# Performance work log

Measured on AMD Instinct MI355X. Metric: run time of the kernel, lower is better.

The kernel has to match this reference:

```python
import jax, jax.numpy as jnp
import numpy as np

N_WIRES = 4
N_LAYERS = 2
B = 16384
EPS = 1e-5


def apply_ry(state, wire, theta):
    # state: (B,2,2,2,2) complex64; theta: scalar or (B,)
    st = jnp.moveaxis(state, wire + 1, 1)
    half = jnp.asarray(theta) * 0.5
    c = jnp.cos(half).reshape(-1, 1, 1, 1).astype(state.dtype)
    s = jnp.sin(half).reshape(-1, 1, 1, 1).astype(state.dtype)
    n0 = c * st[:, 0] - s * st[:, 1]
    n1 = s * st[:, 0] + c * st[:, 1]
    return jnp.moveaxis(jnp.stack([n0, n1], axis=1), 1, wire + 1)


def apply_rz(state, wire, theta):
    st = jnp.moveaxis(state, wire + 1, 1)
    half = jnp.asarray(theta) * 0.5
    c = jnp.cos(half)
    s = jnp.sin(half)
    p0 = (c - 1j * s).reshape(-1, 1, 1, 1).astype(state.dtype)
    p1 = (c + 1j * s).reshape(-1, 1, 1, 1).astype(state.dtype)
    return jnp.moveaxis(jnp.stack([p0 * st[:, 0], p1 * st[:, 1]], axis=1), 1, wire + 1)


def apply_cnot(state, ctrl, tgt):
    st = jnp.moveaxis(state, (ctrl + 1, tgt + 1), (1, 2))
    # flip target where control == 1
    st = jnp.concatenate([st[:, :1], st[:, 1:, ::-1]], axis=1)
    return jnp.moveaxis(st, (1, 2), (ctrl + 1, tgt + 1))


def expect_z(state):
    probs = jnp.real(state * jnp.conj(state))  # (B,2,2,2,2)
    exps = []
    for w in range(N_WIRES):
        p = jnp.moveaxis(probs, w + 1, 1)
        exps.append((p[:, 0] - p[:, 1]).sum(axis=(1, 2, 3)))
    return jnp.stack(exps, axis=-1)  # (B,4)


def quanv(x, qparams):
    bsz = x.shape[0]
    # 2x2 patches in row-major loop order: (B, 196, 4) with [p00,p01,p10,p11]
    patches = x.reshape(bsz, 14, 2, 14, 2).transpose(0, 1, 3, 2, 4).reshape(bsz, 196, 4)
    patches = jnp.transpose(patches, (1, 0, 2))  # (196, B, 4)
    state0 = jnp.zeros((bsz, 2, 2, 2, 2), jnp.complex64).at[:, 0, 0, 0, 0].set(1.0)

    def step(state, vals):
        # NOTE: original code never resets the device between patches -> state carries over
        for i in range(N_WIRES):
            state = apply_ry(state, i, vals[:, i])
        for l in range(N_LAYERS):
            for i in range(N_WIRES):
                state = apply_ry(state, i, qparams[l, i, 0])
                state = apply_rz(state, i, qparams[l, i, 1])
            for i in range(N_WIRES - 1):
                state = apply_cnot(state, i, i + 1)
        return state, expect_z(state)

    _, meas = jax.lax.scan(step, state0, patches)  # (196, B, 4)
    return jnp.transpose(meas, (1, 0, 2)).reshape(bsz, 196 * 4)


def batchnorm(h, g, b):
    # training-mode BatchNorm1d: biased batch statistics
    m = h.mean(axis=0)
    v = h.var(axis=0)
    return g * (h - m) / jnp.sqrt(v + EPS) + b


def setup_inputs() -> dict:
    key = jax.random.key(0)
    ks = jax.random.split(key, 6)
    x = jax.random.uniform(ks[0], (B, 28, 28), dtype=jnp.float32)
    qparams = jax.random.normal(ks[1], (N_LAYERS, N_WIRES, 2), dtype=jnp.float32)
    w1 = jax.random.normal(ks[2], (256, 784), dtype=jnp.float32) * 0.03
    w2 = jax.random.normal(ks[3], (256, 256), dtype=jnp.float32) * 0.05
    w3 = jax.random.normal(ks[4], (10, 256), dtype=jnp.float32) * 0.05
    return {
        "x": x, "qparams": qparams,
        "w1": w1, "b1": jnp.zeros((256,), jnp.float32),
        "g1": jnp.ones((256,), jnp.float32), "be1": jnp.zeros((256,), jnp.float32),
        "w2": w2, "b2": jnp.zeros((256,), jnp.float32),
        "g2": jnp.ones((256,), jnp.float32), "be2": jnp.zeros((256,), jnp.float32),
        "w3": w3, "b3": jnp.zeros((10,), jnp.float32),
    }


def reference(x, qparams, w1, b1, g1, be1, w2, b2, g2, be2, w3, b3):
    feats = quanv(x, qparams)                      # (B, 784)
    h = jax.nn.relu(batchnorm(feats @ w1.T + b1, g1, be1))
    h2 = jax.nn.relu(batchnorm(h @ w2.T + b2, g2, be2)) + h
    return jax.nn.log_softmax(h2 @ w3.T + b3, axis=-1)
```

## Files before the change

kernel.cpp:

```cpp
#include <hip/hip_runtime.h>
#include <math.h>

#define BQ 16384
#define KFP 800
#define NH 256
#define NCLS 10

typedef float f32x2 __attribute__((ext_vector_type(2)));
typedef float f32x4 __attribute__((ext_vector_type(4)));
typedef unsigned int u32x2 __attribute__((ext_vector_type(2)));
typedef __bf16 bf16x8 __attribute__((ext_vector_type(8)));
typedef __bf16 bf16x4 __attribute__((ext_vector_type(4)));


template<int ST>
__device__ __forceinline__ void u_ry(float* sr, float* si, float c, float s) {
#pragma unroll
  for (int i = 0; i < 16; i++) {
    if (i & ST) continue;
    const int j = i | ST;
    const float a0r = sr[i], a0i = si[i], a1r = sr[j], a1i = si[j];
    sr[i] = c * a0r - s * a1r;  si[i] = c * a0i - s * a1i;
    sr[j] = s * a0r + c * a1r;  si[j] = s * a0i + c * a1i;
  }
}
template<int ST>
__device__ __forceinline__ void u_rz(float* sr, float* si, float c, float s) {
#pragma unroll
  for (int i = 0; i < 16; i++) {
    const float pz = (i & ST) ? s : -s;
    const float ar = sr[i], ai = si[i];
    sr[i] = c * ar - pz * ai;
    si[i] = c * ai + pz * ar;
  }
}
template<int SC, int STG>
__device__ __forceinline__ void u_cnot(float* sr, float* si) {
#pragma unroll
  for (int i = 0; i < 16; i++) {
    if (!(i & SC) || (i & STG)) continue;
    const int j = i | STG;
    float t;
    t = sr[i]; sr[i] = sr[j]; sr[j] = t;
    t = si[i]; si[i] = si[j]; si[j] = t;
  }
}

__global__ __launch_bounds__(256) void build_U(const float* __restrict__ qp,
                                               __bf16* __restrict__ Abuf) {
  __shared__ float Ur[16][16], Ui[16][16];
  const int tid = threadIdx.x;
  if (tid < 16) {
    float sr[16], si[16];
#pragma unroll
    for (int i = 0; i < 16; i++) { sr[i] = (i == tid) ? 1.f : 0.f; si[i] = 0.f; }
#pragma unroll
    for (int l = 0; l < 2; l++) {
      { const float t = qp[l*8 + 0] * 0.5f; u_ry<8>(sr, si, cosf(t), sinf(t)); }
      { const float t = qp[l*8 + 1] * 0.5f; u_rz<8>(sr, si, cosf(t), sinf(t)); }
      { const float t = qp[l*8 + 2] * 0.5f; u_ry<4>(sr, si, cosf(t), sinf(t)); }
      { const float t = qp[l*8 + 3] * 0.5f; u_rz<4>(sr, si, cosf(t), sinf(t)); }
      { const float t = qp[l*8 + 4] * 0.5f; u_ry<2>(sr, si, cosf(t), sinf(t)); }
      { const float t = qp[l*8 + 5] * 0.5f; u_rz<2>(sr, si, cosf(t), sinf(t)); }
      { const float t = qp[l*8 + 6] * 0.5f; u_ry<1>(sr, si, cosf(t), sinf(t)); }
      { const float t = qp[l*8 + 7] * 0.5f; u_rz<1>(sr, si, cosf(t), sinf(t)); }
      u_cnot<8, 4>(sr, si);
      u_cnot<4, 2>(sr, si);
      u_cnot<2, 1>(sr, si);
    }
#pragma unroll
    for (int r = 0; r < 16; r++) { Ur[r][tid] = sr[r]; Ui[r][tid] = si[r]; }
  }
  __syncthreads();
  for (int f = tid; f < 2048; f += 256) {
    const int m   = f & 7;
    const int row = (f >> 3) & 15;
    const int kg  = (f >> 7) & 3;
    const int hl  = (f >> 9) & 1;
    const int t   = (f >> 10) & 1;
    const int k   = kg * 8 + m;
    const int ri_o  = (row >> 2) & 1;
    const int amp_o = ((row >> 3) & 1) * 8 + t * 4 + (row & 3);
    const int ri_i  = (k >> 3) & 1;
    const int amp_i = ((k >> 4) & 1) * 8 + (m >> 2) * 4 + (m & 3);
    const float u_r = Ur[amp_o][amp_i], u_i = Ui[amp_o][amp_i];
    float v = (ri_o == 0) ? ((ri_i == 0) ? u_r : -u_i)
                          : ((ri_i == 0) ? u_i : u_r);
    if (hl) {
      const __bf16 hb = (__bf16)v;
      v = v - (float)hb;
    }
    Abuf[f] = (__bf16)v;
  }
}


__device__ __forceinline__ float swz16(float v) {
  return __int_as_float(__builtin_amdgcn_ds_swizzle(__float_as_int(v), 0x401F));
}
__device__ __forceinline__ float pl32(float v, bool r0sel) {
  const u32x2 r = __builtin_amdgcn_permlane32_swap(
      __float_as_uint(v), __float_as_uint(v), false, false);
  return __uint_as_float(r0sel ? r.x : r.y);
}

__global__ __launch_bounds__(256) void quanv_mfma(
    const float* __restrict__ x, const __bf16* __restrict__ Abuf,
    __bf16* __restrict__ feats) {
  const int tid = threadIdx.x;
  const int l = tid & 63;
  const int wv = tid >> 6;
  const int col = l & 15;
  const int kg = l >> 4;
  const int b = blockIdx.x * 64 + wv * 16 + col;
  const float* xb = x + (size_t)b * 784;
  __bf16* fb = feats + (size_t)b * KFP;
  const float sg0 = (l & 32) ? 1.f : -1.f;

  const u32x2 pt = __builtin_amdgcn_permlane32_swap((unsigned)l, (unsigned)l,
                                                    false, false);
  const bool p32r0 = (pt.x == (unsigned)(l ^ 32));

  const bf16x8* Ab = (const bf16x8*)Abuf;
  const bf16x8 A0h = Ab[(0 * 4 + kg) * 16 + col];
  const bf16x8 A0l = Ab[(1 * 4 + kg) * 16 + col];
  const bf16x8 A1h = Ab[(2 * 4 + kg) * 16 + col];
  const bf16x8 A1l = Ab[(3 * 4 + kg) * 16 + col];

  f32x4 c0 = {(kg == 0) ? 1.f : 0.f, 0.f, 0.f, 0.f};
  f32x4 c1 = {0.f, 0.f, 0.f, 0.f};
  const f32x4 z4 = {0.f, 0.f, 0.f, 0.f};

  auto meas = [&](__bf16* dst) {
    const float sq0 = c0.x * c0.x, sq1 = c0.y * c0.y;
    const float sq2 = c0.z * c0.z, sq3 = c0.w * c0.w;
    const float sq4 = c1.x * c1.x, sq5 = c1.y * c1.y;
    const float sq6 = c1.z * c1.z, sq7 = c1.w * c1.w;
    const float s01 = sq0 + sq1, s23 = sq2 + sq3;
    const float s45 = sq4 + sq5, s67 = sq6 + sq7;
    const float d01 = sq0 - sq1, d23 = sq2 - sq3;
    const float d45 = sq4 - sq5, d67 = sq6 - sq7;
    const float z3 = (d01 + d23) + (d45 + d67);
    const float z2 = (s01 - s23) + (s45 - s67);
    const float q03 = s01 + s23, q47 = s45 + s67;
    const float z1 = q03 - q47;
    const float T  = q03 + q47;
    const float z3a = z3 + swz16(z3);
    const float z2a = z2 + swz16(z2);
    const float z1a = z1 + swz16(z1);
    const float Ta  = T + swz16(T);
    const float z3f = z3a + pl32(z3a, p32r0);
    const float z2f = z2a + pl32(z2a, p32r0);
    const float z1f = z1a + pl32(z1a, p32r0);
    const float z0f = sg0 * (pl32(Ta, p32r0) - Ta);
    if (kg == 0) {
      bf16x4 o = {(__bf16)z0f, (__bf16)z1f, (__bf16)z2f, (__bf16)z3f};
      *(bf16x4*)dst = o;
    }
  };

  auto step = [&](float2 t0, float2 t1) {
    const float h0 = t0.x * 0.5f, h1 = t0.y * 0.5f;
    const float h2 = t1.x * 0.5f, h3 = t1.y * 0.5f;
    const float cw0 = __cosf(h0), sw0 = __sinf(h0);
    const float cw1 = __cosf(h1), sw1 = __sinf(h1);
    const float cw2 = __cosf(h2), sw2 = __sinf(h2);
    const float cw3 = __cosf(h3), sw3 = __sinf(h3);

    float S[8] = {c0.x, c0.y, c0.z, c0.w, c1.x, c1.y, c1.z, c1.w};
#pragma unroll
    for (int j = 0; j < 4; j++) {
      const float a = S[j];
      S[j]     = fmaf(-sw1, S[4 + j], cw1 * S[j]);
      S[4 + j] = fmaf( sw1, a,        cw1 * S[4 + j]);
    }
#pragma unroll
    for (int base = 0; base < 8; base += 4)
#pragma unroll
      for (int j = 0; j < 2; j++) {
        const int i0 = base + j, i1 = base + j + 2;
        const float a = S[i0];
        S[i0] = fmaf(-sw2, S[i1], cw2 * S[i0]);
        S[i1] = fmaf( sw2, a,     cw2 * S[i1]);
      }
#pragma unroll
    for (int i0 = 0; i0 < 8; i0 += 2) {
      const float a = S[i0];
      S[i0]     = fmaf(-sw3, S[i0 + 1], cw3 * S[i0]);
      S[i0 + 1] = fmaf( sw3, a,         cw3 * S[i0 + 1]);
    }
    float P[8];
#pragma unroll
    for (int i = 0; i < 8; i++) P[i] = pl32(S[i], p32r0);
    const float ss0 = sg0 * sw0;
#pragma unroll
    for (int i = 0; i < 8; i++) S[i] = fmaf(ss0, P[i], cw0 * S[i]);

    bf16x8 Bh, Bl;
#pragma unroll
    for (int i = 0; i < 8; i++) {
      const __bf16 hb = (__bf16)S[i];
      Bh[i] = hb;
      Bl[i] = (__bf16)(S[i] - (float)hb);
    }

    f32x4 p0 = __builtin_amdgcn_mfma_f32_16x16x32_bf16(A0h, Bh, z4, 0, 0, 0);
    f32x4 q0 = __builtin_amdgcn_mfma_f32_16x16x32_bf16(A0l, Bh, z4, 0, 0, 0);
    q0 = __builtin_amdgcn_mfma_f32_16x16x32_bf16(A0h, Bl, q0, 0, 0, 0);
    f32x4 p1 = __builtin_amdgcn_mfma_f32_16x16x32_bf16(A1h, Bh, z4, 0, 0, 0);
    f32x4 q1 = __builtin_amdgcn_mfma_f32_16x16x32_bf16(A1l, Bh, z4, 0, 0, 0);
    q1 = __builtin_amdgcn_mfma_f32_16x16x32_bf16(A1h, Bl, q1, 0, 0, 0);
    c0 = p0 + q0;
    c1 = p1 + q1;
  };

  float2 t0 = *(const float2*)(xb);
  float2 t1 = *(const float2*)(xb + 28);
  int nrr = 0, ncc = 0;
  {
    const float2 n0 = *(const float2*)(xb + 2);
    const float2 n1 = *(const float2*)(xb + 30);
    step(t0, t1);
    t0 = n0; t1 = n1; ncc = 1; nrr = 0;
  }
  for (int it = 1; it < 196; ++it) {
    int nc = ncc + 1, nr = nrr;
    if (nc == 14) { nc = 0; nr = nrr + 1; }
    const float* np = (it < 195) ? (xb + (2 * nr) * 28 + 2 * nc) : xb;
    const float2 n0 = *(const float2*)np;
    const float2 n1 = *(const float2*)(np + 28);

    meas(fb + (it - 1) * 4);
    step(t0, t1);

    t0 = n0; t1 = n1; ncc = nc; nrr = nr;
  }
  meas(fb + 195 * 4);

  if (kg == 0) {
    *(uint4*)(fb + 784) = (uint4){0, 0, 0, 0};
    *(uint4*)(fb + 792) = (uint4){0, 0, 0, 0};
  }
}

#define GBM 128
#define GBN 64
#define GBK 32

__device__ __forceinline__ void gld16(const void* g, void* l) {
  __builtin_amdgcn_global_load_lds(
      (const __attribute__((address_space(1))) unsigned int*)g,
      (__attribute__((address_space(3))) unsigned int*)l, 16, 0, 0);
}

__global__ __launch_bounds__(256) void gemm_bf16_nt(
    const __bf16* __restrict__ A, const __bf16* __restrict__ B,
    const float* __restrict__ bias, float* __restrict__ C,
    int M, int N, int K) {
  __shared__ char lds[24576];
  const int tid = threadIdx.x;
  const int bm = blockIdx.x * GBM;
  const int bn = blockIdx.y * GBN;
  const int NK = K / GBK;
  const size_t lda = (size_t)K * 2;

  const int srow = tid >> 2;
  const int lc16 = tid & 3;
  const int ag0 = lc16 ^ ((srow >> 1) & 3);
  const int ag1 = lc16 ^ (((srow + 64) >> 1) & 3);
  const char* a0p = (const char*)A + (size_t)(bm + srow) * lda + ag0 * 16;
  const char* a1p = (const char*)A + (size_t)(bm + 64 + srow) * lda + ag1 * 16;
  const char* b0p = (const char*)B + (size_t)(bn + srow) * lda + ag0 * 16;

  const int wid = tid >> 6, lane = tid & 63;
  const int wr = wid >> 1, wc = wid & 1;
  const int ln15 = lane & 15, ln4 = lane >> 4;
  int aoff[4], boff[2];
#pragma unroll
  for (int m = 0; m < 4; m++) {
    const int row = wr * 64 + m * 16 + ln15;
    aoff[m] = row * 64 + ((ln4 ^ ((row >> 1) & 3)) * 16);
  }
#pragma unroll
  for (int n = 0; n < 2; n++) {
    const int row = wc * 32 + n * 16 + ln15;
    boff[n] = 16384 + row * 64 + ((ln4 ^ ((row >> 1) & 3)) * 16);
  }

  f32x4 acc[4][2];
#pragma unroll
  for (int m = 0; m < 4; m++)
#pragma unroll
    for (int n = 0; n < 2; n++) acc[m][n] = (f32x4){0.f, 0.f, 0.f, 0.f};

  auto stage = [&](int buf, int kt) {
    const size_t kb = (size_t)kt * GBK * 2;
    char* as = lds + buf * 8192 + tid * 16;
    char* bs = lds + 16384 + buf * 4096 + tid * 16;
    gld16(a0p + kb, as);
    gld16(a1p + kb, as + 4096);
    gld16(b0p + kb, bs);
  };

  stage(0, 0);
  for (int kt = 0; kt < NK; kt++) {
    __syncthreads();
    if (kt + 1 < NK) stage((kt + 1) & 1, kt + 1);
    const int ab = (kt & 1) * 8192, bb = (kt & 1) * 4096;
    bf16x8 af[4], bfr[2];
#pragma unroll
    for (int m = 0; m < 4; m++) af[m] = *(const bf16x8*)(lds + ab + aoff[m]);
#pragma unroll
    for (int n = 0; n < 2; n++) bfr[n] = *(const bf16x8*)(lds + bb + boff[n]);
#pragma unroll
    for (int m = 0; m < 4; m++)
#pragma unroll
      for (int n = 0; n < 2; n++)
        acc[m][n] = __builtin_amdgcn_mfma_f32_16x16x32_bf16(af[m], bfr[n], acc[m][n], 0, 0, 0);
  }

#pragma unroll
  for (int n = 0; n < 2; n++) {
    const int ccol = bn + wc * 32 + n * 16 + ln15;
    const float bv = bias[ccol];
#pragma unroll
    for (int m = 0; m < 4; m++) {
      const int crow = bm + wr * 64 + m * 16 + ln4 * 4;
#pragma unroll
      for (int r = 0; r < 4; r++)
        C[(size_t)(crow + r) * N + ccol] = acc[m][n][r] + bv;
    }
  }
}

__global__ __launch_bounds__(256) void cvt_pad_w1(const float* __restrict__ w,
                                                  __bf16* __restrict__ o) {
  const int r = blockIdx.x;
  for (int c = threadIdx.x; c < KFP; c += 256)
    o[r * KFP + c] = (c < 784) ? (__bf16)w[r * 784 + c] : (__bf16)0.f;
}
__global__ __launch_bounds__(256) void cvt_w2(const float* __restrict__ w,
                                              __bf16* __restrict__ o) {
  const int i = blockIdx.x * 256 + threadIdx.x;
  o[i] = (__bf16)w[i];
}

__global__ __launch_bounds__(256) void bn_partial(const float* __restrict__ h,
                                                  float* __restrict__ partial) {
  const int blk = blockIdx.x;
  const int t = threadIdx.x;
  const float* p = h + (size_t)blk * 64 * NH + t;
  float s = 0.f, ss = 0.f;
#pragma unroll 4
  for (int r = 0; r < 64; r++) {
    const float v = p[(size_t)r * NH];
    s += v; ss += v * v;
  }
  partial[blk * 512 + t] = s;
  partial[blk * 512 + 256 + t] = ss;
}

__global__ __launch_bounds__(256) void bn_finalize(
    const float* __restrict__ partial, const float* __restrict__ g,
    const float* __restrict__ be, float* __restrict__ ab, float* __restrict__ cb) {
  const int t = threadIdx.x;
  float s = 0.f, ss = 0.f;
  for (int i = 0; i < 256; i++) {
    s += partial[i * 512 + t];
    ss += partial[i * 512 + 256 + t];
  }
  const float mean = s * (1.f / 16384.f);
  const float var = ss * (1.f / 16384.f) - mean * mean;
  const float rstd = rsqrtf(var + 1e-5f);
  const float a = g[t] * rstd;
  ab[t] = a;
  cb[t] = be[t] - mean * a;
}

__global__ __launch_bounds__(256) void bn_relu(float* __restrict__ h,
                                               __bf16* __restrict__ hb,
                                               const float* __restrict__ ab,
                                               const float* __restrict__ cb) {
  const size_t i = (size_t)blockIdx.x * 256 + threadIdx.x;
  float4 v = ((float4*)h)[i];
  const int col = (int)((i * 4) & (NH - 1));
  const float4 a = *(const float4*)(ab + col);
  const float4 c = *(const float4*)(cb + col);
  v.x = fmaxf(v.x * a.x + c.x, 0.f);
  v.y = fmaxf(v.y * a.y + c.y, 0.f);
  v.z = fmaxf(v.z * a.z + c.z, 0.f);
  v.w = fmaxf(v.w * a.w + c.w, 0.f);
  ((float4*)h)[i] = v;
  bf16x4 o = {(__bf16)v.x, (__bf16)v.y, (__bf16)v.z, (__bf16)v.w};
  *(bf16x4*)(hb + i * 4) = o;
}

__global__ __launch_bounds__(256) void bn_relu_res(float* __restrict__ h2,
                                                   const float* __restrict__ h1,
                                                   const float* __restrict__ ab,
                                                   const float* __restrict__ cb) {
  const size_t i = (size_t)blockIdx.x * 256 + threadIdx.x;
  float4 v = ((float4*)h2)[i];
  const float4 rsd = ((const float4*)h1)[i];
  const int col = (int)((i * 4) & (NH - 1));
  const float4 a = *(const float4*)(ab + col);
  const float4 c = *(const float4*)(cb + col);
  v.x = fmaxf(v.x * a.x + c.x, 0.f) + rsd.x;
  v.y = fmaxf(v.y * a.y + c.y, 0.f) + rsd.y;
  v.z = fmaxf(v.z * a.z + c.z, 0.f) + rsd.z;
  v.w = fmaxf(v.w * a.w + c.w, 0.f) + rsd.w;
  ((float4*)h2)[i] = v;
}

__global__ __launch_bounds__(256) void head_kernel(
    const float* __restrict__ h2, const float* __restrict__ w3,
    const float* __restrict__ b3, float* __restrict__ out) {
  __shared__ float w3s[NCLS * NH];
  for (int i = threadIdx.x; i < NCLS * NH; i += 256) w3s[i] = w3[i];
  __syncthreads();

  const int m = blockIdx.x * 256 + threadIdx.x;
  const float* hr = h2 + (size_t)m * NH;
  float acc[NCLS];
#pragma unroll
  for (int n = 0; n < NCLS; n++) acc[n] = b3[n];

  for (int k = 0; k < NH; k += 4) {
    const float4 hv = *(const float4*)(hr + k);
#pragma unroll
    for (int n = 0; n < NCLS; n++) {
      const float4 wv = *(const float4*)&w3s[n * NH + k];
      acc[n] += hv.x * wv.x + hv.y * wv.y + hv.z * wv.z + hv.w * wv.w;
    }
  }

  float mx = acc[0];
#pragma unroll
  for (int n = 1; n < NCLS; n++) mx = fmaxf(mx, acc[n]);
  float se = 0.f;
#pragma unroll
  for (int n = 0; n < NCLS; n++) se += expf(acc[n] - mx);
  const float lse = logf(se) + mx;
#pragma unroll
  for (int n = 0; n < NCLS; n++) out[(size_t)m * NCLS + n] = acc[n] - lse;
}

extern "C" void kernel_launch(void* const* d_in, const int* in_sizes, int n_in,
                              void* d_out, int out_size, void* d_ws, size_t ws_size,
                              hipStream_t stream) {
  const float* x   = (const float*)d_in[0];
  const float* qp  = (const float*)d_in[1];
  const float* w1  = (const float*)d_in[2];
  const float* b1  = (const float*)d_in[3];
  const float* g1  = (const float*)d_in[4];
  const float* be1 = (const float*)d_in[5];
  const float* w2  = (const float*)d_in[6];
  const float* b2  = (const float*)d_in[7];
  const float* g2  = (const float*)d_in[8];
  const float* be2 = (const float*)d_in[9];
  const float* w3  = (const float*)d_in[10];
  const float* b3  = (const float*)d_in[11];
  float* out = (float*)d_out;

  char* w = (char*)d_ws;
  __bf16* feats = (__bf16*)w;
  float*  h1    = (float*)(w + 26214400);
  float*  h2    = (float*)(w + 42991616);
  __bf16* h1b   = (__bf16*)(w + 59768832);
  __bf16* w1b   = (__bf16*)(w + 68157440);
  __bf16* w2b   = (__bf16*)(w + 68567040);
  float*  partial = (float*)(w + 68698112);
  float*  ab1   = (float*)(w + 69222400);
  float*  cb1   = (float*)(w + 69223424);
  float*  ab2   = (float*)(w + 69224448);
  float*  cb2   = (float*)(w + 69225472);
  __bf16* Abuf  = (__bf16*)(w + 69226496);

  build_U<<<1, 256, 0, stream>>>(qp, Abuf);
  cvt_pad_w1<<<256, 256, 0, stream>>>(w1, w1b);
  cvt_w2<<<256, 256, 0, stream>>>(w2, w2b);

  quanv_mfma<<<BQ / 64, 256, 0, stream>>>(x, Abuf, feats);

  gemm_bf16_nt<<<dim3(BQ / GBM, NH / GBN), 256, 0, stream>>>(
      feats, w1b, b1, h1, BQ, NH, KFP);
  bn_partial<<<256, 256, 0, stream>>>(h1, partial);
  bn_finalize<<<1, 256, 0, stream>>>(partial, g1, be1, ab1, cb1);
  bn_relu<<<(BQ * NH / 4) / 256, 256, 0, stream>>>(h1, h1b, ab1, cb1);

  gemm_bf16_nt<<<dim3(BQ / GBM, NH / GBN), 256, 0, stream>>>(
      h1b, w2b, b2, h2, BQ, NH, NH);
  bn_partial<<<256, 256, 0, stream>>>(h2, partial);
  bn_finalize<<<1, 256, 0, stream>>>(partial, g2, be2, ab2, cb2);
  bn_relu_res<<<(BQ * NH / 4) / 256, 256, 0, stream>>>(h2, h1, ab2, cb2);

  head_kernel<<<BQ / 256, 256, 0, stream>>>(h2, w3, b3, out);
}
```

Before: 228.8 us.

## Fuse BN statistics into GEMM epilogue, merge prep and tail kernels

Merges the three weight/unitary prep kernels into one launch and folds the batchnorm sum and sum-of-squares into the GEMM epilogue using LDS reduction plus global atomics. This removes the separate bn_partial passes over h1/h2. The second BN+ReLU, residual add and classifier head become one tail kernel that reads the bf16 h1 as the residual, so the h2 round trip is dropped. The quanv loop now computes the trig for the next patch after the current step and packs bf16 with perm instructions. Risks: atomic float accumulation makes the statistics order-dependent, and the residual now uses a bf16-rounded h1.

```diff
diff --git a/kernel.cpp b/kernel.cpp
--- a/kernel.cpp
+++ b/kernel.cpp
@@ -6,9 +6,9 @@
 #define NH 256
 #define NCLS 10
 
-typedef float f32x2 __attribute__((ext_vector_type(2)));
 typedef float f32x4 __attribute__((ext_vector_type(4)));
 typedef unsigned int u32x2 __attribute__((ext_vector_type(2)));
+typedef unsigned int u32x4 __attribute__((ext_vector_type(4)));
 typedef __bf16 bf16x8 __attribute__((ext_vector_type(8)));
 typedef __bf16 bf16x4 __attribute__((ext_vector_type(4)));
 
@@ -46,51 +46,70 @@
   }
 }
 
-__global__ __launch_bounds__(256) void build_U(const float* __restrict__ qp,
-                                               __bf16* __restrict__ Abuf) {
-  __shared__ float Ur[16][16], Ui[16][16];
+__global__ __launch_bounds__(256) void prep_kernel(
+    const float* __restrict__ qp, const float* __restrict__ w1,
+    const float* __restrict__ w2, __bf16* __restrict__ Abuf,
+    __bf16* __restrict__ w1b, __bf16* __restrict__ w2b,
+    float* __restrict__ gs1, float* __restrict__ gs2) {
+  const int bid = blockIdx.x;
   const int tid = threadIdx.x;
-  if (tid < 16) {
-    float sr[16], si[16];
-#pragma unroll
-    for (int i = 0; i < 16; i++) { sr[i] = (i == tid) ? 1.f : 0.f; si[i] = 0.f; }
-#pragma unroll
-    for (int l = 0; l < 2; l++) {
-      { const float t = qp[l*8 + 0] * 0.5f; u_ry<8>(sr, si, cosf(t), sinf(t)); }
-      { const float t = qp[l*8 + 1] * 0.5f; u_rz<8>(sr, si, cosf(t), sinf(t)); }
-      { const float t = qp[l*8 + 2] * 0.5f; u_ry<4>(sr, si, cosf(t), sinf(t)); }
-      { const float t = qp[l*8 + 3] * 0.5f; u_rz<4>(sr, si, cosf(t), sinf(t)); }
-      { const float t = qp[l*8 + 4] * 0.5f; u_ry<2>(sr, si, cosf(t), sinf(t)); }
-      { const float t = qp[l*8 + 5] * 0.5f; u_rz<2>(sr, si, cosf(t), sinf(t)); }
-      { const float t = qp[l*8 + 6] * 0.5f; u_ry<1>(sr, si, cosf(t), sinf(t)); }
-      { const float t = qp[l*8 + 7] * 0.5f; u_rz<1>(sr, si, cosf(t), sinf(t)); }
-      u_cnot<8, 4>(sr, si);
-      u_cnot<4, 2>(sr, si);
-      u_cnot<2, 1>(sr, si);
-    }
-#pragma unroll
-    for (int r = 0; r < 16; r++) { Ur[r][tid] = sr[r]; Ui[r][tid] = si[r]; }
-  }
-  __syncthreads();
-  for (int f = tid; f < 2048; f += 256) {
-    const int m   = f & 7;
-    const int row = (f >> 3) & 15;
-    const int kg  = (f >> 7) & 3;
-    const int hl  = (f >> 9) & 1;
-    const int t   = (f >> 10) & 1;
-    const int k   = kg * 8 + m;
-    const int ri_o  = (row >> 2) & 1;
-    const int amp_o = ((row >> 3) & 1) * 8 + t * 4 + (row & 3);
-    const int ri_i  = (k >> 3) & 1;
-    const int amp_i = ((k >> 4) & 1) * 8 + (m >> 2) * 4 + (m & 3);
-    const float u_r = Ur[amp_o][amp_i], u_i = Ui[amp_o][amp_i];
-    float v = (ri_o == 0) ? ((ri_i == 0) ? u_r : -u_i)
-                          : ((ri_i == 0) ? u_i : u_r);
-    if (hl) {
-      const __bf16 hb = (__bf16)v;
-      v = v - (float)hb;
-    }
-    Abuf[f] = (__bf16)v;
+  if (bid == 0) {
+    gs1[tid] = 0.f; gs1[256 + tid] = 0.f;
+    gs2[tid] = 0.f; gs2[256 + tid] = 0.f;
+    __shared__ float Ur[16][16], Ui[16][16];
+    if (tid < 16) {
+      float sr[16], si[16];
+#pragma unroll
+      for (int i = 0; i < 16; i++) { sr[i] = (i == tid) ? 1.f : 0.f; si[i] = 0.f; }
+#pragma unroll
+      for (int l = 0; l < 2; l++) {
+        { const float t = qp[l*8 + 0] * 0.5f; u_ry<8>(sr, si, cosf(t), sinf(t)); }
+        { const float t = qp[l*8 + 1] * 0.5f; u_rz<8>(sr, si, cosf(t), sinf(t)); }
+        { const float t = qp[l*8 + 2] * 0.5f; u_ry<4>(sr, si, cosf(t), sinf(t)); }
+        { const float t = qp[l*8 + 3] * 0.5f; u_rz<4>(sr, si, cosf(t), sinf(t)); }
+        { const float t = qp[l*8 + 4] * 0.5f; u_ry<2>(sr, si, cosf(t), sinf(t)); }
+        { const float t = qp[l*8 + 5] * 0.5f; u_rz<2>(sr, si, cosf(t), sinf(t)); }
+        { const float t = qp[l*8 + 6] * 0.5f; u_ry<1>(sr, si, cosf(t), sinf(t)); }
+        { const float t = qp[l*8 + 7] * 0.5f; u_rz<1>(sr, si, cosf(t), sinf(t)); }
+        u_cnot<8, 4>(sr, si);
+        u_cnot<4, 2>(sr, si);
+        u_cnot<2, 1>(sr, si);
+      }
+#pragma unroll
+      for (int r = 0; r < 16; r++) { Ur[r][tid] = sr[r]; Ui[r][tid] = si[r]; }
+    }
+    __syncthreads();
+    for (int f = tid; f < 2048; f += 256) {
+      const int m   = f & 7;
+      const int row = (f >> 3) & 15;
+      const int kg  = (f >> 7) & 3;
+      const int hl  = (f >> 9) & 1;
+      const int t   = (f >> 10) & 1;
+      const int k   = kg * 8 + m;
+      const int ri_o  = (row >> 2) & 1;
+      const int amp_o = ((row >> 3) & 1) * 8 + t * 4 + (row & 3);
+      const int ri_i  = (k >> 3) & 1;
+      const int amp_i = ((k >> 4) & 1) * 8 + (m >> 2) * 4 + (m & 3);
+      const float u_r = Ur[amp_o][amp_i], u_i = Ui[amp_o][amp_i];
+      float v = (ri_o == 0) ? ((ri_i == 0) ? u_r : -u_i)
+                            : ((ri_i == 0) ? u_i : u_r);
+      if (hl) {
+        const __bf16 hb = (__bf16)v;
+        v = v - (float)hb;
+      }
+      Abuf[f] = (__bf16)v;
+    }
+  } else if (bid <= 256) {
+    const int r = bid - 1;
+    for (int c = tid; c < KFP; c += 256)
+      w1b[r * KFP + c] = (c < 784) ? (__bf16)w1[r * 784 + c] : (__bf16)0.f;
+  } else {
+    const int base = (bid - 257) * 2048 + tid * 8;
+    const float4 v0 = *(const float4*)(w2 + base);
+    const float4 v1 = *(const float4*)(w2 + base + 4);
+    bf16x8 o = {(__bf16)v0.x, (__bf16)v0.y, (__bf16)v0.z, (__bf16)v0.w,
+                (__bf16)v1.x, (__bf16)v1.y, (__bf16)v1.z, (__bf16)v1.w};
+    *(bf16x8*)(w2b + base) = o;
   }
 }
 
@@ -130,6 +149,16 @@
   f32x4 c0 = {(kg == 0) ? 1.f : 0.f, 0.f, 0.f, 0.f};
   f32x4 c1 = {0.f, 0.f, 0.f, 0.f};
   const f32x4 z4 = {0.f, 0.f, 0.f, 0.f};
+
+  float cw[4], sw[4];
+  auto trig = [&](float2 a, float2 b2) {
+    const float h0 = a.x * 0.5f, h1 = a.y * 0.5f;
+    const float h2 = b2.x * 0.5f, h3 = b2.y * 0.5f;
+    cw[0] = __cosf(h0); sw[0] = __sinf(h0);
+    cw[1] = __cosf(h1); sw[1] = __sinf(h1);
+    cw[2] = __cosf(h2); sw[2] = __sinf(h2);
+    cw[3] = __cosf(h3); sw[3] = __sinf(h3);
+  };
 
   auto meas = [&](__bf16* dst) {
     const float sq0 = c0.x * c0.x, sq1 = c0.y * c0.y;
@@ -159,20 +188,13 @@
     }
   };
 
-  auto step = [&](float2 t0, float2 t1) {
-    const float h0 = t0.x * 0.5f, h1 = t0.y * 0.5f;
-    const float h2 = t1.x * 0.5f, h3 = t1.y * 0.5f;
-    const float cw0 = __cosf(h0), sw0 = __sinf(h0);
-    const float cw1 = __cosf(h1), sw1 = __sinf(h1);
-    const float cw2 = __cosf(h2), sw2 = __sinf(h2);
-    const float cw3 = __cosf(h3), sw3 = __sinf(h3);
-
+  auto step = [&]() {
     float S[8] = {c0.x, c0.y, c0.z, c0.w, c1.x, c1.y, c1.z, c1.w};
 #pragma unroll
     for (int j = 0; j < 4; j++) {
       const float a = S[j];
-      S[j]     = fmaf(-sw1, S[4 + j], cw1 * S[j]);
-      S[4 + j] = fmaf( sw1, a,        cw1 * S[4 + j]);
+      S[j]     = fmaf(-sw[1], S[4 + j], cw[1] * S[j]);
+      S[4 + j] = fmaf( sw[1], a,        cw[1] * S[4 + j]);
     }
 #pragma unroll
     for (int base = 0; base < 8; base += 4)
@@ -180,62 +202,70 @@
       for (int j = 0; j < 2; j++) {
         const int i0 = base + j, i1 = base + j + 2;
         const float a = S[i0];
-        S[i0] = fmaf(-sw2, S[i1], cw2 * S[i0]);
-        S[i1] = fmaf( sw2, a,     cw2 * S[i1]);
+        S[i0] = fmaf(-sw[2], S[i1], cw[2] * S[i0]);
+        S[i1] = fmaf( sw[2], a,     cw[2] * S[i1]);
       }
 #pragma unroll
     for (int i0 = 0; i0 < 8; i0 += 2) {
       const float a = S[i0];
-      S[i0]     = fmaf(-sw3, S[i0 + 1], cw3 * S[i0]);
-      S[i0 + 1] = fmaf( sw3, a,         cw3 * S[i0 + 1]);
+      S[i0]     = fmaf(-sw[3], S[i0 + 1], cw[3] * S[i0]);
+      S[i0 + 1] = fmaf( sw[3], a,         cw[3] * S[i0 + 1]);
     }
     float P[8];
 #pragma unroll
     for (int i = 0; i < 8; i++) P[i] = pl32(S[i], p32r0);
-    const float ss0 = sg0 * sw0;
-#pragma unroll
-    for (int i = 0; i < 8; i++) S[i] = fmaf(ss0, P[i], cw0 * S[i]);
-
-    bf16x8 Bh, Bl;
+    const float ss0 = sg0 * sw[0];
+#pragma unroll
+    for (int i = 0; i < 8; i++) S[i] = fmaf(ss0, P[i], cw[0] * S[i]);
+
+    unsigned sb[8], lb[8];
 #pragma unroll
     for (int i = 0; i < 8; i++) {
-      const __bf16 hb = (__bf16)S[i];
-      Bh[i] = hb;
-      Bl[i] = (__bf16)(S[i] - (float)hb);
-    }
-
-    f32x4 p0 = __builtin_amdgcn_mfma_f32_16x16x32_bf16(A0h, Bh, z4, 0, 0, 0);
-    f32x4 q0 = __builtin_amdgcn_mfma_f32_16x16x32_bf16(A0l, Bh, z4, 0, 0, 0);
-    q0 = __builtin_amdgcn_mfma_f32_16x16x32_bf16(A0h, Bl, q0, 0, 0, 0);
-    f32x4 p1 = __builtin_amdgcn_mfma_f32_16x16x32_bf16(A1h, Bh, z4, 0, 0, 0);
-    f32x4 q1 = __builtin_amdgcn_mfma_f32_16x16x32_bf16(A1l, Bh, z4, 0, 0, 0);
-    q1 = __builtin_amdgcn_mfma_f32_16x16x32_bf16(A1h, Bl, q1, 0, 0, 0);
-    c0 = p0 + q0;
-    c1 = p1 + q1;
+      sb[i] = __float_as_uint(S[i]);
+      lb[i] = __float_as_uint(S[i] - __uint_as_float(sb[i] & 0xFFFF0000u));
+    }
+    u32x4 bh, bl;
+#pragma unroll
+    for (int j = 0; j < 4; j++) {
+      bh[j] = __builtin_amdgcn_perm(sb[2 * j + 1], sb[2 * j], 0x07060302u);
+      bl[j] = __builtin_amdgcn_perm(lb[2 * j + 1], lb[2 * j], 0x07060302u);
+    }
+    const bf16x8 Bh = __builtin_bit_cast(bf16x8, bh);
+    const bf16x8 Bl = __builtin_bit_cast(bf16x8, bl);
+
+    const f32x4 p0 = __builtin_amdgcn_mfma_f32_16x16x32_bf16(A0h, Bh, z4, 0, 0, 0);
+    const f32x4 q0 = __builtin_amdgcn_mfma_f32_16x16x32_bf16(A0l, Bh, z4, 0, 0, 0);
+    const f32x4 r0 = __builtin_amdgcn_mfma_f32_16x16x32_bf16(A0h, Bl, z4, 0, 0, 0);
+    const f32x4 p1 = __builtin_amdgcn_mfma_f32_16x16x32_bf16(A1h, Bh, z4, 0, 0, 0);
+    const f32x4 q1 = __builtin_amdgcn_mfma_f32_16x16x32_bf16(A1l, Bh, z4, 0, 0, 0);
+    const f32x4 r1 = __builtin_amdgcn_mfma_f32_16x16x32_bf16(A1h, Bl, z4, 0, 0, 0);
+    c0 = (p0 + q0) + r0;
+    c1 = (p1 + q1) + r1;
   };
 
-  float2 t0 = *(const float2*)(xb);
-  float2 t1 = *(const float2*)(xb + 28);
-  int nrr = 0, ncc = 0;
   {
-    const float2 n0 = *(const float2*)(xb + 2);
-    const float2 n1 = *(const float2*)(xb + 30);
-    step(t0, t1);
-    t0 = n0; t1 = n1; ncc = 1; nrr = 0;
-  }
-  for (int it = 1; it < 196; ++it) {
-    int nc = ncc + 1, nr = nrr;
-    if (nc == 14) { nc = 0; nr = nrr + 1; }
-    const float* np = (it < 195) ? (xb + (2 * nr) * 28 + 2 * nc) : xb;
+    const float2 a0 = *(const float2*)(xb);
+    const float2 a1 = *(const float2*)(xb + 28);
+    trig(a0, a1);
+  }
+  float2 t0 = *(const float2*)(xb + 2);
+  float2 t1 = *(const float2*)(xb + 30);
+  int nrr = 0, ncc = 2;
+  __bf16* fp = fb;
+
+  for (int it = 0; it < 196; ++it) {
+    const float* np = (it < 194) ? (xb + 56 * nrr + 2 * ncc) : xb;
     const float2 n0 = *(const float2*)np;
     const float2 n1 = *(const float2*)(np + 28);
-
-    meas(fb + (it - 1) * 4);
-    step(t0, t1);
-
-    t0 = n0; t1 = n1; ncc = nc; nrr = nr;
-  }
-  meas(fb + 195 * 4);
+    ncc++;
+    if (ncc == 14) { ncc = 0; nrr++; }
+
+    if (it > 0) { meas(fp); fp += 4; }
+    step();
+    trig(t0, t1);
+    t0 = n0; t1 = n1;
+  }
+  meas(fp);
 
   if (kg == 0) {
     *(uint4*)(fb + 784) = (uint4){0, 0, 0, 0};
@@ -256,7 +286,7 @@
 __global__ __launch_bounds__(256) void gemm_bf16_nt(
     const __bf16* __restrict__ A, const __bf16* __restrict__ B,
     const float* __restrict__ bias, float* __restrict__ C,
-    int M, int N, int K) {
+    int M, int N, int K, float* __restrict__ gstats) {
   __shared__ char lds[24576];
   const int tid = threadIdx.x;
   const int bm = blockIdx.x * GBM;
@@ -319,56 +349,52 @@
         acc[m][n] = __builtin_amdgcn_mfma_f32_16x16x32_bf16(af[m], bfr[n], acc[m][n], 0, 0, 0);
   }
 
+  float csum[2], csq[2];
 #pragma unroll
   for (int n = 0; n < 2; n++) {
     const int ccol = bn + wc * 32 + n * 16 + ln15;
     const float bv = bias[ccol];
+    float s = 0.f, ss = 0.f;
 #pragma unroll
     for (int m = 0; m < 4; m++) {
       const int crow = bm + wr * 64 + m * 16 + ln4 * 4;
 #pragma unroll
-      for (int r = 0; r < 4; r++)
-        C[(size_t)(crow + r) * N + ccol] = acc[m][n][r] + bv;
-    }
-  }
-}
-
-__global__ __launch_bounds__(256) void cvt_pad_w1(const float* __restrict__ w,
-                                                  __bf16* __restrict__ o) {
-  const int r = blockIdx.x;
-  for (int c = threadIdx.x; c < KFP; c += 256)
-    o[r * KFP + c] = (c < 784) ? (__bf16)w[r * 784 + c] : (__bf16)0.f;
-}
-__global__ __launch_bounds__(256) void cvt_w2(const float* __restrict__ w,
-                                              __bf16* __restrict__ o) {
-  const int i = blockIdx.x * 256 + threadIdx.x;
-  o[i] = (__bf16)w[i];
-}
-
-__global__ __launch_bounds__(256) void bn_partial(const float* __restrict__ h,
-                                                  float* __restrict__ partial) {
-  const int blk = blockIdx.x;
-  const int t = threadIdx.x;
-  const float* p = h + (size_t)blk * 64 * NH + t;
-  float s = 0.f, ss = 0.f;
-#pragma unroll 4
-  for (int r = 0; r < 64; r++) {
-    const float v = p[(size_t)r * NH];
-    s += v; ss += v * v;
-  }
-  partial[blk * 512 + t] = s;
-  partial[blk * 512 + 256 + t] = ss;
-}
-
-__global__ __launch_bounds__(256) void bn_finalize(
-    const float* __restrict__ partial, const float* __restrict__ g,
+      for (int r = 0; r < 4; r++) {
+        const float v = acc[m][n][r] + bv;
+        C[(size_t)(crow + r) * N + ccol] = v;
+        s += v; ss += v * v;
+      }
+    }
+    csum[n] = s; csq[n] = ss;
+  }
+  __syncthreads();
+  float* sred = (float*)lds;
+#pragma unroll
+  for (int n = 0; n < 2; n++) {
+    const int slot = wid * 128 + ln4 * 32 + n * 16 + ln15;
+    sred[slot] = csum[n];
+    sred[512 + slot] = csq[n];
+  }
+  __syncthreads();
+  if (tid < 128) {
+    const int colb = tid & 63, which = tid >> 6;
+    const int wcc = colb >> 5, c31 = colb & 31;
+    float a = 0.f;
+    const int base = which * 512 + c31;
+#pragma unroll
+    for (int w2_ = 0; w2_ < 2; w2_++)
+#pragma unroll
+      for (int l4 = 0; l4 < 4; l4++)
+        a += sred[base + (w2_ * 2 + wcc) * 128 + l4 * 32];
+    atomicAdd(&gstats[(bn + colb) * 2 + which], a);
+  }
+}
+
+__global__ __launch_bounds__(256) void bn_finalize_g(
+    const float* __restrict__ gstats, const float* __restrict__ g,
     const float* __restrict__ be, float* __restrict__ ab, float* __restrict__ cb) {
   const int t = threadIdx.x;
-  float s = 0.f, ss = 0.f;
-  for (int i = 0; i < 256; i++) {
-    s += partial[i * 512 + t];
-    ss += partial[i * 512 + 256 + t];
-  }
+  const float s = gstats[t * 2], ss = gstats[t * 2 + 1];
   const float mean = s * (1.f / 16384.f);
   const float var = ss * (1.f / 16384.f) - mean * mean;
   const float rstd = rsqrtf(var + 1e-5f);
@@ -377,60 +403,54 @@
   cb[t] = be[t] - mean * a;
 }
 
-__global__ __launch_bounds__(256) void bn_relu(float* __restrict__ h,
-                                               __bf16* __restrict__ hb,
-                                               const float* __restrict__ ab,
-                                               const float* __restrict__ cb) {
+__global__ __launch_bounds__(256) void bn_relu_cvt(
+    const float* __restrict__ h, __bf16* __restrict__ hb,
+    const float* __restrict__ ab, const float* __restrict__ cb) {
   const size_t i = (size_t)blockIdx.x * 256 + threadIdx.x;
-  float4 v = ((float4*)h)[i];
+  const float4 v = ((const float4*)h)[i];
   const int col = (int)((i * 4) & (NH - 1));
   const float4 a = *(const float4*)(ab + col);
   const float4 c = *(const float4*)(cb + col);
-  v.x = fmaxf(v.x * a.x + c.x, 0.f);
-  v.y = fmaxf(v.y * a.y + c.y, 0.f);
-  v.z = fmaxf(v.z * a.z + c.z, 0.f);
-  v.w = fmaxf(v.w * a.w + c.w, 0.f);
-  ((float4*)h)[i] = v;
-  bf16x4 o = {(__bf16)v.x, (__bf16)v.y, (__bf16)v.z, (__bf16)v.w};
+  bf16x4 o = {(__bf16)fmaxf(fmaf(v.x, a.x, c.x), 0.f),
+              (__bf16)fmaxf(fmaf(v.y, a.y, c.y), 0.f),
+              (__bf16)fmaxf(fmaf(v.z, a.z, c.z), 0.f),
+              (__bf16)fmaxf(fmaf(v.w, a.w, c.w), 0.f)};
   *(bf16x4*)(hb + i * 4) = o;
 }
 
-__global__ __launch_bounds__(256) void bn_relu_res(float* __restrict__ h2,
-                                                   const float* __restrict__ h1,
-                                                   const float* __restrict__ ab,
-                                                   const float* __restrict__ cb) {
-  const size_t i = (size_t)blockIdx.x * 256 + threadIdx.x;
-  float4 v = ((float4*)h2)[i];
-  const float4 rsd = ((const float4*)h1)[i];
-  const int col = (int)((i * 4) & (NH - 1));
-  const float4 a = *(const float4*)(ab + col);
-  const float4 c = *(const float4*)(cb + col);
-  v.x = fmaxf(v.x * a.x + c.x, 0.f) + rsd.x;
-  v.y = fmaxf(v.y * a.y + c.y, 0.f) + rsd.y;
-  v.z = fmaxf(v.z * a.z + c.z, 0.f) + rsd.z;
-  v.w = fmaxf(v.w * a.w + c.w, 0.f) + rsd.w;
-  ((float4*)h2)[i] = v;
-}
-
-__global__ __launch_bounds__(256) void head_kernel(
-    const float* __restrict__ h2, const float* __restrict__ w3,
-    const float* __restrict__ b3, float* __restrict__ out) {
+__global__ __launch_bounds__(256) void tail_fused(
+    const float* __restrict__ h2p, const __bf16* __restrict__ h1b,
+    const float* __restrict__ ab, const float* __restrict__ cb,
+    const float* __restrict__ w3, const float* __restrict__ b3,
+    float* __restrict__ out) {
   __shared__ float w3s[NCLS * NH];
+  __shared__ float as[NH], cs[NH];
   for (int i = threadIdx.x; i < NCLS * NH; i += 256) w3s[i] = w3[i];
+  as[threadIdx.x] = ab[threadIdx.x];
+  cs[threadIdx.x] = cb[threadIdx.x];
   __syncthreads();
 
   const int m = blockIdx.x * 256 + threadIdx.x;
-  const float* hr = h2 + (size_t)m * NH;
+  const float* hr = h2p + (size_t)m * NH;
+  const __bf16* rr = h1b + (size_t)m * NH;
   float acc[NCLS];
 #pragma unroll
   for (int n = 0; n < NCLS; n++) acc[n] = b3[n];
 
-  for (int k = 0; k < NH; k += 4) {
-    const float4 hv = *(const float4*)(hr + k);
+  for (int k = 0; k < NH; k += 8) {
+    const float4 hv0 = *(const float4*)(hr + k);
+    const float4 hv1 = *(const float4*)(hr + k + 4);
+    const bf16x8 rv = *(const bf16x8*)(rr + k);
+    float v[8] = {hv0.x, hv0.y, hv0.z, hv0.w, hv1.x, hv1.y, hv1.z, hv1.w};
+#pragma unroll
+    for (int j = 0; j < 8; j++)
+      v[j] = fmaxf(fmaf(v[j], as[k + j], cs[k + j]), 0.f) + (float)rv[j];
 #pragma unroll
     for (int n = 0; n < NCLS; n++) {
-      const float4 wv = *(const float4*)&w3s[n * NH + k];
-      acc[n] += hv.x * wv.x + hv.y * wv.y + hv.z * wv.z + hv.w * wv.w;
+      float d = 0.f;
+#pragma unroll
+      for (int j = 0; j < 8; j++) d = fmaf(v[j], w3s[n * NH + k + j], d);
+      acc[n] += d;
     }
   }
 
@@ -465,34 +485,29 @@
   char* w = (char*)d_ws;
   __bf16* feats = (__bf16*)w;
   float*  h1    = (float*)(w + 26214400);
-  float*  h2    = (float*)(w + 42991616);
+  float*  h2p   = (float*)(w + 42991616);
   __bf16* h1b   = (__bf16*)(w + 59768832);
   __bf16* w1b   = (__bf16*)(w + 68157440);
   __bf16* w2b   = (__bf16*)(w + 68567040);
-  float*  partial = (float*)(w + 68698112);
-  float*  ab1   = (float*)(w + 69222400);
-  float*  cb1   = (float*)(w + 69223424);
-  float*  ab2   = (float*)(w + 69224448);
-  float*  cb2   = (float*)(w + 69225472);
-  __bf16* Abuf  = (__bf16*)(w + 69226496);
-
-  build_U<<<1, 256, 0, stream>>>(qp, Abuf);
-  cvt_pad_w1<<<256, 256, 0, stream>>>(w1, w1b);
-  cvt_w2<<<256, 256, 0, stream>>>(w2, w2b);
-
+  float*  gs1   = (float*)(w + 68698112);
+  float*  gs2   = (float*)(w + 68700160);
+  float*  ab1   = (float*)(w + 68702208);
+  float*  cb1   = (float*)(w + 68703232);
+  float*  ab2   = (float*)(w + 68704256);
+  float*  cb2   = (float*)(w + 68705280);
+  __bf16* Abuf  = (__bf16*)(w + 68706304);
+
+  prep_kernel<<<289, 256, 0, stream>>>(qp, w1, w2, Abuf, w1b, w2b, gs1, gs2);
   quanv_mfma<<<BQ / 64, 256, 0, stream>>>(x, Abuf, feats);
 
   gemm_bf16_nt<<<dim3(BQ / GBM, NH / GBN), 256, 0, stream>>>(
-      feats, w1b, b1, h1, BQ, NH, KFP);
-  bn_partial<<<256, 256, 0, stream>>>(h1, partial);
-  bn_finalize<<<1, 256, 0, stream>>>(partial, g1, be1, ab1, cb1);
-  bn_relu<<<(BQ * NH / 4) / 256, 256, 0, stream>>>(h1, h1b, ab1, cb1);
+      feats, w1b, b1, h1, BQ, NH, KFP, gs1);
+  bn_finalize_g<<<1, 256, 0, stream>>>(gs1, g1, be1, ab1, cb1);
+  bn_relu_cvt<<<(BQ * NH / 4) / 256, 256, 0, stream>>>(h1, h1b, ab1, cb1);
 
   gemm_bf16_nt<<<dim3(BQ / GBM, NH / GBN), 256, 0, stream>>>(
-      h1b, w2b, b2, h2, BQ, NH, NH);
-  bn_partial<<<256, 256, 0, stream>>>(h2, partial);
-  bn_finalize<<<1, 256, 0, stream>>>(partial, g2, be2, ab2, cb2);
-  bn_relu_res<<<(BQ * NH / 4) / 256, 256, 0, stream>>>(h2, h1, ab2, cb2);
-
-  head_kernel<<<BQ / 256, 256, 0, stream>>>(h2, w3, b3, out);
-}
+      h1b, w2b, b2, h2p, BQ, NH, NH, gs2);
+  bn_finalize_g<<<1, 256, 0, stream>>>(gs2, g2, be2, ab2, cb2);
+
+  tail_fused<<<BQ / 256, 256, 0, stream>>>(h2p, h1b, ab2, cb2, w3, b3, out);
+}
```

New measurement: 201.0 us. 1.14x faster.
